# Kernel optimization log

Measured on AMD Instinct MI355X. Metric: run time of the kernel, lower is better.

## Reference

```python
import jax, jax.numpy as jnp
import numpy as np

ROUTING_ITERATIONS = 3


def squash(x):
    # squared norm over the capsule output dim
    sq = jnp.sum(x * x, axis=-1, keepdims=True)
    scale = sq / (1.0 + sq)
    return scale * x / jnp.sqrt(sq)


def setup_inputs() -> dict:
    key = jax.random.key(0)
    k1, k2 = jax.random.split(key)
    B, N, IN_C, K, OUT_C = 256, 1152, 8, 10, 16
    u = jax.random.normal(k1, (B, N, IN_C), dtype=jnp.float32)
    W = jax.random.normal(k2, (K, N, IN_C, OUT_C), dtype=jnp.float32)
    return {"u": u, "W": W}


def reference(u, W):
    # u: [B, N, in_c]; W: [K, N, in_c, out_c]
    # torch: u_hat = matmul(u[None,:,:,None,:], W[:,None]) -> [K, B, N, 1, out_c]
    u_hat = jnp.einsum('bni,knio->kbno', u, W)  # [K, B, N, out_c]
    b_ij = jnp.zeros_like(u_hat)
    v_j = None
    for it in range(ROUTING_ITERATIONS):
        c_ij = jax.nn.softmax(b_ij, axis=2)               # softmax over N, per out_c channel
        s_j = jnp.sum(c_ij * u_hat, axis=2, keepdims=True)  # [K, B, 1, out_c]
        v_j = squash(s_j)
        if it < ROUTING_ITERATIONS - 1:
            a_ij = jnp.sum(u_hat * v_j, axis=-1, keepdims=True)  # [K, B, N, 1]
            b_ij = b_ij + a_ij
    # match torch output shape [K, B, 1, 1, out_c]
    return v_j[:, :, :, None, :]
```

## Files before the change

### kernel.cpp

```cpp
#include <hip/hip_runtime.h>
#include <hip/hip_fp16.h>

#define Bsz 256
#define Nn  1152
#define Kk  10
#define NT  384
#define NW  6
#define S4  1160

#define W_ELEMS (Kk*Nn*128)
#define U_ELEMS (Bsz*Nn*8)

static __device__ __forceinline__ unsigned pkh2(float x, float y) {
    __half2 h = __floats2half2_rn(x, y);
    return *reinterpret_cast<unsigned*>(&h);
}
static __device__ __forceinline__ float2 uph2(unsigned v) {
    __half2 h;
    *reinterpret_cast<unsigned*>(&h) = v;
    return __half22float2(h);
}
static __device__ __forceinline__ void up8(const uint4 q, float f[8]) {
    float2 a = uph2(q.x), b = uph2(q.y), c = uph2(q.z), d = uph2(q.w);
    f[0]=a.x; f[1]=a.y; f[2]=b.x; f[3]=b.y; f[4]=c.x; f[5]=c.y; f[6]=d.x; f[7]=d.y;
}

__global__ void cvt_kernel(const float* __restrict__ W, const float* __restrict__ u,
                           __half2* __restrict__ Wh, __half2* __restrict__ uh) {
    const int idx = blockIdx.x * blockDim.x + threadIdx.x;
    const int wg = W_ELEMS / 8;
    const float4* p;
    __half2* o;
    if (idx < wg) {
        p = (const float4*)W + (size_t)idx * 2;
        o = Wh + (size_t)idx * 4;
    } else {
        const int j = idx - wg;
        p = (const float4*)u + (size_t)j * 2;
        o = uh + (size_t)j * 4;
    }
    const float4 a = p[0], b = p[1];
    o[0] = __floats2half2_rn(a.x, a.y);
    o[1] = __floats2half2_rn(a.z, a.w);
    o[2] = __floats2half2_rn(b.x, b.y);
    o[3] = __floats2half2_rn(b.z, b.w);
}

template<bool HALF>
__global__ __launch_bounds__(NT, 6)
void digitcaps_kernel(const float* __restrict__ u32, const float* __restrict__ W32,
                      const __half* __restrict__ uh, const __half* __restrict__ Wh,
                      float* __restrict__ out)
{
    const int t    = threadIdx.x;
    const int lane = t & 63;
    const int wav  = t >> 6;
    const int b    = blockIdx.x;
    const int k    = blockIdx.y;

    __shared__ unsigned       uhS[8 * S4];
    __shared__ unsigned short cS[Nn];
    __shared__ float          redS[NW * 17];
    __shared__ __align__(16) float vS[16];
    __shared__ float          mS[1];

    {
        const int oh   = t & 1;
        const int nsub = t >> 1;
        for (int r = 0; r < 6; ++r) {
            const int n = r * 192 + nsub;
            float ua[8];
            if (HALF) {
                const uint4 qa = *(const uint4*)(uh + ((size_t)b * Nn + n) * 8);
                up8(qa, ua);
            } else {
                const float4* up0 = (const float4*)(u32 + ((size_t)b * Nn + n) * 8);
                const float4 x0 = up0[0], x1 = up0[1];
                ua[0]=x0.x; ua[1]=x0.y; ua[2]=x0.z; ua[3]=x0.w;
                ua[4]=x1.x; ua[5]=x1.y; ua[6]=x1.z; ua[7]=x1.w;
            }
            float a0[8];
            #pragma unroll
            for (int o = 0; o < 8; ++o) a0[o] = 0.f;
            #pragma unroll
            for (int i = 0; i < 8; ++i) {
                float wv[8];
                if (HALF) {
                    const uint4 qw = *(const uint4*)(Wh + ((size_t)(k * Nn + n)) * 128 + i * 16 + oh * 8);
                    up8(qw, wv);
                } else {
                    const float4* wp = (const float4*)(W32 + ((size_t)k * Nn + n) * 128) + oh * 2 + i * 4;
                    const float4 w0 = wp[0], w1 = wp[1];
                    wv[0]=w0.x; wv[1]=w0.y; wv[2]=w0.z; wv[3]=w0.w;
                    wv[4]=w1.x; wv[5]=w1.y; wv[6]=w1.z; wv[7]=w1.w;
                }
                const float x = ua[i];
                #pragma unroll
                for (int o = 0; o < 8; ++o) a0[o] += x * wv[o];
            }
            #pragma unroll
            for (int jj = 0; jj < 4; ++jj)
                uhS[(oh * 4 + jj) * S4 + n] = pkh2(a0[2*jj], a0[2*jj+1]);
        }
    }
    __syncthreads();

    float lg[3] = {0.f, 0.f, 0.f};
    float vv[16];
    const int j_s = lane & 7;
    const int g_s = lane >> 3;

    for (int it = 0; it < 3; ++it) {
        if (it > 0) {
            #pragma unroll
            for (int r = 0; r < 3; ++r) {
                const int n = t + r * NT;
                float acc = 0.f;
                #pragma unroll
                for (int j = 0; j < 8; ++j) {
                    const float2 f = uph2(uhS[j * S4 + n]);
                    acc += f.x * vv[2*j] + f.y * vv[2*j+1];
                }
                lg[r] += acc;
            }
            float m = fmaxf(fmaxf(lg[0], lg[1]), lg[2]);
            #pragma unroll
            for (int off = 1; off <= 32; off <<= 1)
                m = fmaxf(m, __shfl_xor(m, off));
            if (lane == 0) redS[wav] = m;
            __syncthreads();
            if (t == 0) {
                float mm = redS[0];
                #pragma unroll
                for (int w = 1; w < NW; ++w) mm = fmaxf(mm, redS[w]);
                mS[0] = mm;
            }
            __syncthreads();
            m = mS[0];
            #pragma unroll
            for (int r = 0; r < 3; ++r) {
                const __half eh = __float2half(__expf(lg[r] - m));
                cS[t + r * NT] = *reinterpret_cast<const unsigned short*>(&eh);
            }
            __syncthreads();
        }

        float2 sp = {0.f, 0.f};
        float dp = 0.f;
        #pragma unroll
        for (int cc = 0; cc < 24; ++cc) {
            const int n = cc * 48 + wav * 8 + g_s;
            float c;
            if (it == 0) c = 1.f;
            else {
                const unsigned short eb = cS[n];
                c = __half2float(*reinterpret_cast<const __half*>(&eb));
            }
            const float2 f = uph2(uhS[j_s * S4 + n]);
            sp.x += c * f.x;
            sp.y += c * f.y;
            dp   += c;
        }
        #pragma unroll
        for (int off = 8; off <= 32; off <<= 1) {
            sp.x += __shfl_xor(sp.x, off);
            sp.y += __shfl_xor(sp.y, off);
            dp   += __shfl_xor(dp,   off);
        }
        if (lane < 8) {
            redS[wav * 17 + 2*j_s    ] = sp.x;
            redS[wav * 17 + 2*j_s + 1] = sp.y;
        }
        if (lane == 0) redS[wav * 17 + 16] = dp;
        __syncthreads();

        if (t < 16) {
            const int o = t;
            float s = 0.f, d = 0.f;
            #pragma unroll
            for (int w = 0; w < NW; ++w) {
                s += redS[w * 17 + o];
                d += redS[w * 17 + 16];
            }
            s /= d;
            float s2 = s * s;
            #pragma unroll
            for (int off = 1; off <= 8; off <<= 1) s2 += __shfl_xor(s2, off);
            const float scale = (s2 / (1.f + s2)) * rsqrtf(fmaxf(s2, 1e-30f));
            const float v = s * scale;
            vS[o] = v;
            if (it == 2) out[((size_t)k * Bsz + b) * 16 + o] = v;
        }
        if (it == 2) break;
        __syncthreads();

        {
            const float4* vp = (const float4*)vS;
            #pragma unroll
            for (int q4 = 0; q4 < 4; ++q4)
                *(float4*)&vv[4*q4] = vp[q4];
        }
    }
}

extern "C" void kernel_launch(void* const* d_in, const int* in_sizes, int n_in,
                              void* d_out, int out_size, void* d_ws, size_t ws_size,
                              hipStream_t stream) {
    const float* u = (const float*)d_in[0];
    const float* W = (const float*)d_in[1];
    float* out = (float*)d_out;
    const size_t need = (size_t)(W_ELEMS + U_ELEMS) * sizeof(__half);
    if (ws_size >= need) {
        __half* Wh = (__half*)d_ws;
        __half* uh = (__half*)((char*)d_ws + (size_t)W_ELEMS * sizeof(__half));
        cvt_kernel<<<dim3((W_ELEMS + U_ELEMS) / 8 / 256), dim3(256), 0, stream>>>(
            W, u, (__half2*)Wh, (__half2*)uh);
        digitcaps_kernel<true><<<dim3(256, 10), dim3(NT), 0, stream>>>(
            nullptr, nullptr, uh, Wh, out);
    } else {
        digitcaps_kernel<false><<<dim3(256, 10), dim3(NT), 0, stream>>>(
            u, W, nullptr, nullptr, out);
    }
}
```

Baseline: 128.5 us.

## Use packed fp16 dot2 instructions and redundant per-wave squash to cut syncs

Replaces fp16-to-fp32 unpack plus FMA sequences with v_dot2 (fdot2) on packed half pairs in the u_hat projection, the agreement dot product and the weighted sum, using byte permutes to pair operands. Every wave now computes the squash redundantly from the shared partial sums, and the softmax max is reduced by all threads, removing two barriers and the vS shared-memory round trip per iteration. In exchange v_j is rounded to fp16 before the agreement dot, which loses some precision, and there are extra perm instructions plus duplicated work across waves.

```diff
diff --git a/kernel.cpp b/kernel.cpp
--- a/kernel.cpp
+++ b/kernel.cpp
@@ -11,6 +11,8 @@
 #define W_ELEMS (Kk*Nn*128)
 #define U_ELEMS (Bsz*Nn*8)
 
+typedef _Float16 hf2_t __attribute__((ext_vector_type(2)));
+
 static __device__ __forceinline__ unsigned pkh2(float x, float y) {
     __half2 h = __floats2half2_rn(x, y);
     return *reinterpret_cast<unsigned*>(&h);
@@ -20,10 +22,15 @@
     *reinterpret_cast<unsigned*>(&h) = v;
     return __half22float2(h);
 }
-static __device__ __forceinline__ void up8(const uint4 q, float f[8]) {
-    float2 a = uph2(q.x), b = uph2(q.y), c = uph2(q.z), d = uph2(q.w);
-    f[0]=a.x; f[1]=a.y; f[2]=b.x; f[3]=b.y; f[4]=c.x; f[5]=c.y; f[6]=d.x; f[7]=d.y;
-}
+static __device__ __forceinline__ float fdot2u(unsigned a, unsigned b, float c) {
+    union { unsigned u; hf2_t h; } A, B;
+    A.u = a; B.u = b;
+    return __builtin_amdgcn_fdot2(A.h, B.h, c, false);
+}
+
+#define PERM_LO 0x01000504u
+#define PERM_HI 0x03020706u
+#define ONE2    0x3C003C00u
 
 __global__ void cvt_kernel(const float* __restrict__ W, const float* __restrict__ u,
                            __half2* __restrict__ Wh, __half2* __restrict__ uh) {
@@ -61,42 +68,51 @@
     __shared__ unsigned       uhS[8 * S4];
     __shared__ unsigned short cS[Nn];
     __shared__ float          redS[NW * 17];
-    __shared__ __align__(16) float vS[16];
-    __shared__ float          mS[1];
+    __shared__ float          mxS[NW];
 
     {
         const int oh   = t & 1;
         const int nsub = t >> 1;
         for (int r = 0; r < 6; ++r) {
             const int n = r * 192 + nsub;
-            float ua[8];
+            float a0[8];
+            #pragma unroll
+            for (int o = 0; o < 8; ++o) a0[o] = 0.f;
             if (HALF) {
-                const uint4 qa = *(const uint4*)(uh + ((size_t)b * Nn + n) * 8);
-                up8(qa, ua);
+                const uint4 uq = *(const uint4*)(uh + ((size_t)b * Nn + n) * 8);
+                const unsigned uw[4] = {uq.x, uq.y, uq.z, uq.w};
+                const __half* wbase = Wh + ((size_t)(k * Nn + n)) * 128 + oh * 8;
+                #pragma unroll
+                for (int p = 0; p < 4; ++p) {
+                    const uint4 qa = *(const uint4*)(wbase + (2 * p    ) * 16);
+                    const uint4 qb = *(const uint4*)(wbase + (2 * p + 1) * 16);
+                    const unsigned aw[4] = {qa.x, qa.y, qa.z, qa.w};
+                    const unsigned bw[4] = {qb.x, qb.y, qb.z, qb.w};
+                    #pragma unroll
+                    for (int jj = 0; jj < 4; ++jj) {
+                        const unsigned wl = __builtin_amdgcn_perm(aw[jj], bw[jj], PERM_LO);
+                        const unsigned wh = __builtin_amdgcn_perm(aw[jj], bw[jj], PERM_HI);
+                        a0[2*jj]   = fdot2u(wl, uw[p], a0[2*jj]);
+                        a0[2*jj+1] = fdot2u(wh, uw[p], a0[2*jj+1]);
+                    }
+                }
             } else {
+                float ua[8];
                 const float4* up0 = (const float4*)(u32 + ((size_t)b * Nn + n) * 8);
                 const float4 x0 = up0[0], x1 = up0[1];
                 ua[0]=x0.x; ua[1]=x0.y; ua[2]=x0.z; ua[3]=x0.w;
                 ua[4]=x1.x; ua[5]=x1.y; ua[6]=x1.z; ua[7]=x1.w;
-            }
-            float a0[8];
-            #pragma unroll
-            for (int o = 0; o < 8; ++o) a0[o] = 0.f;
-            #pragma unroll
-            for (int i = 0; i < 8; ++i) {
-                float wv[8];
-                if (HALF) {
-                    const uint4 qw = *(const uint4*)(Wh + ((size_t)(k * Nn + n)) * 128 + i * 16 + oh * 8);
-                    up8(qw, wv);
-                } else {
+                #pragma unroll
+                for (int i = 0; i < 8; ++i) {
                     const float4* wp = (const float4*)(W32 + ((size_t)k * Nn + n) * 128) + oh * 2 + i * 4;
                     const float4 w0 = wp[0], w1 = wp[1];
+                    float wv[8];
                     wv[0]=w0.x; wv[1]=w0.y; wv[2]=w0.z; wv[3]=w0.w;
                     wv[4]=w1.x; wv[5]=w1.y; wv[6]=w1.z; wv[7]=w1.w;
+                    const float x = ua[i];
+                    #pragma unroll
+                    for (int o = 0; o < 8; ++o) a0[o] += x * wv[o];
                 }
-                const float x = ua[i];
-                #pragma unroll
-                for (int o = 0; o < 8; ++o) a0[o] += x * wv[o];
             }
             #pragma unroll
             for (int jj = 0; jj < 4; ++jj)
@@ -106,7 +122,7 @@
     __syncthreads();
 
     float lg[3] = {0.f, 0.f, 0.f};
-    float vv[16];
+    unsigned vh[8];
     const int j_s = lane & 7;
     const int g_s = lane >> 3;
 
@@ -117,29 +133,22 @@
                 const int n = t + r * NT;
                 float acc = 0.f;
                 #pragma unroll
-                for (int j = 0; j < 8; ++j) {
-                    const float2 f = uph2(uhS[j * S4 + n]);
-                    acc += f.x * vv[2*j] + f.y * vv[2*j+1];
-                }
+                for (int j = 0; j < 8; ++j)
+                    acc = fdot2u(uhS[j * S4 + n], vh[j], acc);
                 lg[r] += acc;
             }
             float m = fmaxf(fmaxf(lg[0], lg[1]), lg[2]);
             #pragma unroll
             for (int off = 1; off <= 32; off <<= 1)
                 m = fmaxf(m, __shfl_xor(m, off));
-            if (lane == 0) redS[wav] = m;
+            if (lane == 0) mxS[wav] = m;
             __syncthreads();
-            if (t == 0) {
-                float mm = redS[0];
-                #pragma unroll
-                for (int w = 1; w < NW; ++w) mm = fmaxf(mm, redS[w]);
-                mS[0] = mm;
-            }
-            __syncthreads();
-            m = mS[0];
+            float mm = mxS[0];
+            #pragma unroll
+            for (int w = 1; w < NW; ++w) mm = fmaxf(mm, mxS[w]);
             #pragma unroll
             for (int r = 0; r < 3; ++r) {
-                const __half eh = __float2half(__expf(lg[r] - m));
+                const __half eh = __float2half(__expf(lg[r] - mm));
                 cS[t + r * NT] = *reinterpret_cast<const unsigned short*>(&eh);
             }
             __syncthreads();
@@ -148,18 +157,19 @@
         float2 sp = {0.f, 0.f};
         float dp = 0.f;
         #pragma unroll
-        for (int cc = 0; cc < 24; ++cc) {
-            const int n = cc * 48 + wav * 8 + g_s;
-            float c;
-            if (it == 0) c = 1.f;
-            else {
-                const unsigned short eb = cS[n];
-                c = __half2float(*reinterpret_cast<const __half*>(&eb));
-            }
-            const float2 f = uph2(uhS[j_s * S4 + n]);
-            sp.x += c * f.x;
-            sp.y += c * f.y;
-            dp   += c;
+        for (int c2 = 0; c2 < 12; ++c2) {
+            const int n0 = c2 * 96 + wav * 8 + g_s;
+            const int n1 = n0 + 48;
+            unsigned cp;
+            if (it == 0) cp = ONE2;
+            else cp = (unsigned)cS[n0] | ((unsigned)cS[n1] << 16);
+            const unsigned q0 = uhS[j_s * S4 + n0];
+            const unsigned q1 = uhS[j_s * S4 + n1];
+            const unsigned px = __builtin_amdgcn_perm(q0, q1, PERM_LO);
+            const unsigned py = __builtin_amdgcn_perm(q0, q1, PERM_HI);
+            sp.x = fdot2u(px, cp, sp.x);
+            sp.y = fdot2u(py, cp, sp.y);
+            dp   = fdot2u(cp, ONE2, dp);
         }
         #pragma unroll
         for (int off = 8; off <= 32; off <<= 1) {
@@ -174,8 +184,8 @@
         if (lane == 0) redS[wav * 17 + 16] = dp;
         __syncthreads();
 
-        if (t < 16) {
-            const int o = t;
+        {
+            const int o = lane & 15;
             float s = 0.f, d = 0.f;
             #pragma unroll
             for (int w = 0; w < NW; ++w) {
@@ -188,17 +198,14 @@
             for (int off = 1; off <= 8; off <<= 1) s2 += __shfl_xor(s2, off);
             const float scale = (s2 / (1.f + s2)) * rsqrtf(fmaxf(s2, 1e-30f));
             const float v = s * scale;
-            vS[o] = v;
-            if (it == 2) out[((size_t)k * Bsz + b) * 16 + o] = v;
-        }
-        if (it == 2) break;
-        __syncthreads();
-
-        {
-            const float4* vp = (const float4*)vS;
-            #pragma unroll
-            for (int q4 = 0; q4 < 4; ++q4)
-                *(float4*)&vv[4*q4] = vp[q4];
+            if (it == 2) {
+                if (wav == 0 && lane < 16)
+                    out[((size_t)k * Bsz + b) * 16 + lane] = v;
+            } else {
+                #pragma unroll
+                for (int j = 0; j < 8; ++j)
+                    vh[j] = pkh2(__shfl(v, 2*j), __shfl(v, 2*j + 1));
+            }
         }
     }
 }
```

Result: no change. 127.3 us (-0.9%).
